# Kernel optimization log

Measured on AMD Instinct MI355X. Metric: run time of the kernel, lower is better.

The kernel has to match this reference:

```python
import jax, jax.numpy as jnp
import numpy as np

TOP_K = 4
N_GROUP = 8
TOPK_GROUP = 4
SCALE = 1.0

B, S, H, I, E = 2, 1024, 1024, 512, 32
SHARED_I = I * 2  # n_shared_experts = 2


def setup_inputs() -> dict:
    key = jax.random.key(0)
    ks = jax.random.split(key, 9)
    return {
        "hidden_states": jax.random.normal(ks[0], (B, S, H), jnp.float32),
        "gate_w": jax.random.normal(ks[1], (E, H), jnp.float32) * 0.02,
        "gate_bias": jnp.zeros((E,), jnp.float32),
        "gate_proj": jax.random.normal(ks[2], (E, I, H), jnp.float32) * 0.02,
        "up_proj": jax.random.normal(ks[3], (E, I, H), jnp.float32) * 0.02,
        "down_proj": jax.random.normal(ks[4], (E, H, I), jnp.float32) * 0.02,
        "shared_gate_w": jax.random.normal(ks[5], (SHARED_I, H), jnp.float32) * 0.02,
        "shared_up_w": jax.random.normal(ks[6], (SHARED_I, H), jnp.float32) * 0.02,
        "shared_down_w": jax.random.normal(ks[7], (H, SHARED_I), jnp.float32) * 0.02,
    }


def reference(hidden_states, gate_w, gate_bias, gate_proj, up_proj, down_proj,
              shared_gate_w, shared_up_w, shared_down_w):
    b, s, h = hidden_states.shape
    e = gate_w.shape[0]
    x = hidden_states.reshape(-1, h)            # (T, H)
    t = x.shape[0]

    # ---- gating (DeepSeek-V3 grouped sigmoid routing) ----
    logits = x @ gate_w.T                       # (T, E)
    scores = jax.nn.sigmoid(logits)
    sfc = scores + gate_bias[None, :]           # scores_for_choice
    # per-group score = sum of top-2 experts in group
    group_scores = jax.lax.top_k(sfc.reshape(t, N_GROUP, -1), 2)[0].sum(-1)  # (T, G)
    _, gidx = jax.lax.top_k(group_scores, TOPK_GROUP)                        # (T, topk_group)
    gmask = jax.nn.one_hot(gidx, N_GROUP, dtype=sfc.dtype).sum(1)            # (T, G)
    smask = jnp.repeat(gmask, e // N_GROUP, axis=1)                          # (T, E)
    tmp = jnp.where(smask > 0, sfc, 0.0)
    _, topk_idx = jax.lax.top_k(tmp, TOP_K)                                  # (T, K)
    topk_w = jnp.take_along_axis(scores, topk_idx, axis=1)                   # (T, K)
    topk_w = topk_w / (topk_w.sum(-1, keepdims=True) + 1e-20)                # norm_topk_prob
    topk_w = topk_w * SCALE

    # ---- routed experts (dense combine-weight formulation) ----
    comb = jnp.zeros((t, e), x.dtype).at[jnp.arange(t)[:, None], topk_idx].add(topk_w)  # (T, E)
    g = jnp.einsum('th,eih->eti', x, gate_proj)   # (E, T, I)
    u = jnp.einsum('th,eih->eti', x, up_proj)     # (E, T, I)
    a = jax.nn.silu(g) * u
    a = a * comb.T[:, :, None]                    # scale before down-proj to skip zero experts
    out = jnp.einsum('eti,ehi->th', a, down_proj) # (T, H)

    # ---- shared experts ----
    sg = x @ shared_gate_w.T
    su = x @ shared_up_w.T
    out = out + (jax.nn.silu(sg) * su) @ shared_down_w.T

    return out.reshape(b, s, h)
```

## Files before the change

kernel.cpp:

```cpp
#include <hip/hip_runtime.h>
#include <hip/hip_bf16.h>
#include <cstdint>
#include <cstddef>

#define H_DIM 1024
#define I_DIM 512
#define E_NUM 32
#define SHARED_I_DIM 1024
#define TOPK 4
#define NGROUP 8
#define TOPKG 4
#define GT 8

typedef __attribute__((ext_vector_type(8))) short bf16x8;
typedef __attribute__((ext_vector_type(4))) float f32x4;
typedef __attribute__((ext_vector_type(8))) unsigned short u16x8;

__device__ inline unsigned short f2bf(float f) {
    __hip_bfloat16 h = __float2bfloat16(f);
    return *reinterpret_cast<unsigned short*>(&h);
}
__device__ inline float bf2f(unsigned short u) {
    union { unsigned int u; float f; } w;
    w.u = ((unsigned int)u) << 16;
    return w.f;
}

__device__ inline int laddr(int row, int chunk) {
    return row * 32 + ((chunk ^ ((row >> 1) & 3)) << 3);
}

__global__ __launch_bounds__(256) void gate_kernel(const float* __restrict__ x,
                                                   const float* __restrict__ gw,
                                                   float* __restrict__ logits_out,
                                                   unsigned short* __restrict__ x_bf,
                                                   int* __restrict__ cnt) {
    int tb = blockIdx.x;
    int tid = threadIdx.x;
    if (tb == 0 && tid < 64) cnt[tid] = 0;
    __shared__ float xs[GT][H_DIM];
    __shared__ float ps[8][GT][E_NUM];
    const float* xsrc = x + (size_t)tb * GT * H_DIM;
    for (int i = tid; i < GT * H_DIM / 4; i += 256)
        ((float4*)&xs[0][0])[i] = ((const float4*)xsrc)[i];
    __syncthreads();
    {
        unsigned short* dst = x_bf + (size_t)tb * GT * H_DIM;
#pragma unroll
        for (int i = 0; i < GT * H_DIM / 8 / 256; ++i) {
            int idx = i * 256 + tid;
            const float* s = &xs[0][0] + idx * 8;
            u16x8 v;
            v[0] = f2bf(s[0]); v[1] = f2bf(s[1]); v[2] = f2bf(s[2]); v[3] = f2bf(s[3]);
            v[4] = f2bf(s[4]); v[5] = f2bf(s[5]); v[6] = f2bf(s[6]); v[7] = f2bf(s[7]);
            *(u16x8*)(dst + idx * 8) = v;
        }
    }
    int e = tid & 31, part = tid >> 5;
    const float* wrow = gw + (size_t)e * H_DIM + part * 128;
    float acc[GT] = {};
    for (int c0 = 0; c0 < 128; c0 += 32) {
        float w[32];
#pragma unroll
        for (int c = 0; c < 32; c++) w[c] = wrow[c0 + c];
#pragma unroll
        for (int t = 0; t < GT; t++) {
#pragma unroll
            for (int c = 0; c < 32; c++)
                acc[t] += w[c] * xs[t][part * 128 + c0 + c];
        }
    }
#pragma unroll
    for (int t = 0; t < GT; t++) ps[part][t][e] = acc[t];
    __syncthreads();
    {
        int t = tid >> 5, ee = tid & 31;
        float s = 0.f;
#pragma unroll
        for (int p = 0; p < 8; p++) s += ps[p][t][ee];
        logits_out[((size_t)tb * GT + t) * E_NUM + ee] = s;
    }
}

__global__ void select_kernel(const float* __restrict__ logits, const float* __restrict__ gb,
                              int* __restrict__ topk_e, float* __restrict__ topk_w,
                              int* __restrict__ cnt, int T) {
    int t = blockIdx.x * blockDim.x + threadIdx.x;
    if (t >= T) return;
    float scores[E_NUM], sfc[E_NUM];
#pragma unroll
    for (int i = 0; i < E_NUM; i++) {
        float l = logits[(size_t)t * E_NUM + i];
        float s = 1.f / (1.f + expf(-l));
        scores[i] = s;
        sfc[i] = s + gb[i];
    }
    float gs[NGROUP];
#pragma unroll
    for (int g = 0; g < NGROUP; g++) {
        float m1 = -1e30f, m2 = -1e30f;
#pragma unroll
        for (int j = 0; j < 4; j++) {
            float v = sfc[g * 4 + j];
            if (v > m1) { m2 = m1; m1 = v; }
            else if (v > m2) { m2 = v; }
        }
        gs[g] = m1 + m2;
    }
    unsigned gmask = 0;
    for (int r = 0; r < TOPKG; r++) {
        int best = 0; float bv = -1e30f;
#pragma unroll
        for (int g = 0; g < NGROUP; g++)
            if (!((gmask >> g) & 1u) && gs[g] > bv) { bv = gs[g]; best = g; }
        gmask |= 1u << best;
    }
    unsigned cmask = 0;
    int eidx[TOPK]; float ew[TOPK]; float sum = 0.f;
    for (int r = 0; r < TOPK; r++) {
        int best = 0; float bv = -1e30f; float bsc = 0.f;
#pragma unroll
        for (int i = 0; i < E_NUM; i++) {
            float v = ((gmask >> (i >> 2)) & 1u) ? sfc[i] : 0.0f;
            if (!((cmask >> i) & 1u) && v > bv) { bv = v; best = i; bsc = scores[i]; }
        }
        cmask |= 1u << best;
        eidx[r] = best; ew[r] = bsc; sum += bsc;
    }
    float inv = 1.f / (sum + 1e-20f);
#pragma unroll
    for (int k = 0; k < TOPK; k++) {
        topk_e[t * TOPK + k] = eidx[k];
        topk_w[t * TOPK + k] = ew[k] * inv;
        atomicAdd(&cnt[eidx[k]], 1);
    }
}

__global__ void scan_kernel(const int* __restrict__ cnt, int* __restrict__ off) {
    if (threadIdx.x == 0) {
        int a = 0;
        for (int e = 0; e < E_NUM; e++) { off[e] = a; a += cnt[e]; }
        off[E_NUM] = a;
    }
}

__global__ void bin_kernel(const int* __restrict__ topk_e, const float* __restrict__ topk_w,
                           const int* __restrict__ off, int* __restrict__ cnt2,
                           int* __restrict__ slot_token, float* __restrict__ slot_w,
                           int* __restrict__ slot_of, int total) {
    int i = blockIdx.x * blockDim.x + threadIdx.x;
    if (i >= total) return;
    int e = topk_e[i];
    float w = topk_w[i];
    int pos = atomicAdd(&cnt2[e], 1);
    int slot = off[e] + pos;
    slot_token[slot] = i >> 2;
    slot_w[slot] = w;
    slot_of[i] = slot;
}

__global__ __launch_bounds__(256) void combine_kernel(const unsigned short* __restrict__ out_slot,
                                                      const int* __restrict__ slot_of,
                                                      float* __restrict__ out) {
    int t = blockIdx.x;
    int h = threadIdx.x * 4;
    int s0 = slot_of[t * TOPK + 0], s1 = slot_of[t * TOPK + 1];
    int s2 = slot_of[t * TOPK + 2], s3 = slot_of[t * TOPK + 3];
    ushort4 a = *(const ushort4*)(out_slot + (size_t)s0 * H_DIM + h);
    ushort4 b = *(const ushort4*)(out_slot + (size_t)s1 * H_DIM + h);
    ushort4 c = *(const ushort4*)(out_slot + (size_t)s2 * H_DIM + h);
    ushort4 d = *(const ushort4*)(out_slot + (size_t)s3 * H_DIM + h);
    float4 o = *(float4*)(out + (size_t)t * H_DIM + h);
    o.x += bf2f(a.x) + bf2f(b.x) + bf2f(c.x) + bf2f(d.x);
    o.y += bf2f(a.y) + bf2f(b.y) + bf2f(c.y) + bf2f(d.y);
    o.z += bf2f(a.z) + bf2f(b.z) + bf2f(c.z) + bf2f(d.z);
    o.w += bf2f(a.w) + bf2f(b.w) + bf2f(c.w) + bf2f(d.w);
    *(float4*)(out + (size_t)t * H_DIM + h) = o;
}

template <bool STAGE1>
__global__ __launch_bounds__(512, 2) void moe_gemm(
    const unsigned short* __restrict__ Axr, const unsigned short* __restrict__ Axs,
    const float* __restrict__ B1r_, const float* __restrict__ B2r_,
    const float* __restrict__ B1s_, const float* __restrict__ B2s_,
    void* __restrict__ Dr, void* __restrict__ Ds,
    const int* __restrict__ slot_token, const float* __restrict__ slot_w,
    const int* __restrict__ cnt, const int* __restrict__ off_arr, int T) {
    constexpr bool DUAL = STAGE1;
    int e = blockIdx.x, itile = blockIdx.y, mtile = blockIdx.z;
    bool sh = (e == E_NUM);
    int NI = STAGE1 ? (sh ? 16 : 8) : 16;
    if (itile >= NI) return;
    int count = sh ? T : cnt[e];
    int base = sh ? 0 : off_arr[e];
    if (mtile * 256 >= count) return;
    const int K = STAGE1 ? H_DIM : (sh ? SHARED_I_DIM : I_DIM);

    __shared__ __align__(16) unsigned short As[2][256 * 32];
    __shared__ __align__(16) unsigned short Bs1[2][64 * 32];
    __shared__ __align__(16) unsigned short Bs2[2][DUAL ? 64 * 32 : 8];

    int tid = threadIdx.x, lane = tid & 63, wid = tid >> 6;

    int as_row = tid >> 1, as_c0 = (tid & 1) * 2;
    int am = mtile * 256 + as_row;
    int amc = (am < count) ? am : 0;
    const unsigned short* Abase;
    size_t arow;
    if constexpr (STAGE1) {
        Abase = Axr;
        arow = sh ? (size_t)amc : (size_t)slot_token[base + amc];
    } else {
        Abase = sh ? Axs : Axr;
        arow = sh ? (size_t)amc : (size_t)(base + amc);
    }
    const unsigned short* Ga = Abase + arow * K + as_c0 * 8;

    int bs_row = tid >> 3;
    int brow = itile * 64 + bs_row;
    int bwr = laddr(bs_row, (tid & 7) >> 1) + (tid & 1) * 4;
    const float* Gb1;
    const float* Gb2 = nullptr;
    if constexpr (STAGE1) {
        Gb1 = (sh ? B1s_ : (B1r_ + (size_t)e * (I_DIM * H_DIM))) + (size_t)brow * K + (tid & 7) * 4;
        Gb2 = (sh ? B2s_ : (B2r_ + (size_t)e * (I_DIM * H_DIM))) + (size_t)brow * K + (tid & 7) * 4;
    } else {
        Gb1 = (sh ? B1s_ : (B1r_ + (size_t)e * (H_DIM * I_DIM))) + (size_t)brow * K + (tid & 7) * 4;
    }

    f32x4 acc1[4][2] = {};
    f32x4 acc2[DUAL ? 4 : 1][2] = {};

    int wrow = (wid >> 1) * 64, wcol = (wid & 1) * 32;
    int frow = lane & 15, fch = lane >> 4;

    u16x8 a00, a01, a10, a11;
    float4 b10, b20, b11, b21;

    auto loadS = [&](u16x8& a0, u16x8& a1, float4& b1v, float4& b2v, int ks) {
        int k0 = ks << 5;
        a0 = *(const u16x8*)(Ga + k0);
        a1 = *(const u16x8*)(Ga + k0 + 8);
        b1v = *(const float4*)(Gb1 + k0);
        if constexpr (DUAL) b2v = *(const float4*)(Gb2 + k0);
    };
    auto writeS = [&](int buf, u16x8 a0, u16x8 a1, float4 b1v, float4 b2v) {
        *(u16x8*)(&As[buf][laddr(as_row, as_c0)]) = a0;
        *(u16x8*)(&As[buf][laddr(as_row, as_c0 + 1)]) = a1;
        ushort4 s;
        s.x = f2bf(b1v.x); s.y = f2bf(b1v.y); s.z = f2bf(b1v.z); s.w = f2bf(b1v.w);
        *(ushort4*)(&Bs1[buf][bwr]) = s;
        if constexpr (DUAL) {
            ushort4 s2;
            s2.x = f2bf(b2v.x); s2.y = f2bf(b2v.y); s2.z = f2bf(b2v.z); s2.w = f2bf(b2v.w);
            *(ushort4*)(&Bs2[buf][bwr]) = s2;
        }
    };
    auto compute = [&](int buf) {
        bf16x8 af[4], b1[2], b2[DUAL ? 2 : 1];
#pragma unroll
        for (int nf = 0; nf < 2; nf++)
            b1[nf] = *(const bf16x8*)(&Bs1[buf][laddr(wcol + nf * 16 + frow, fch)]);
        if constexpr (DUAL) {
#pragma unroll
            for (int nf = 0; nf < 2; nf++)
                b2[nf] = *(const bf16x8*)(&Bs2[buf][laddr(wcol + nf * 16 + frow, fch)]);
        }
#pragma unroll
        for (int mf = 0; mf < 4; mf++)
            af[mf] = *(const bf16x8*)(&As[buf][laddr(wrow + mf * 16 + frow, fch)]);
#pragma unroll
        for (int mf = 0; mf < 4; mf++)
#pragma unroll
            for (int nf = 0; nf < 2; nf++) {
                acc1[mf][nf] = __builtin_amdgcn_mfma_f32_16x16x32_bf16(af[mf], b1[nf], acc1[mf][nf], 0, 0, 0);
                if constexpr (DUAL)
                    acc2[mf][nf] = __builtin_amdgcn_mfma_f32_16x16x32_bf16(af[mf], b2[nf], acc2[mf][nf], 0, 0, 0);
            }
    };

    const int NK = K >> 5;
    loadS(a00, a01, b10, b20, 0);
    loadS(a10, a11, b11, b21, 1);
    writeS(0, a00, a01, b10, b20);
    loadS(a00, a01, b10, b20, 2);
    __syncthreads();
    for (int it = 0; it < NK; it += 2) {
        writeS(1, a10, a11, b11, b21);
        if (it + 3 < NK) loadS(a10, a11, b11, b21, it + 3);
        compute(0);
        __syncthreads();
        if (it + 2 < NK) {
            writeS(0, a00, a01, b10, b20);
            if (it + 4 < NK) loadS(a00, a01, b10, b20, it + 4);
        }
        compute(1);
        if (it + 2 < NK) __syncthreads();
    }

#pragma unroll
    for (int mf = 0; mf < 4; mf++)
#pragma unroll
        for (int nf = 0; nf < 2; nf++)
#pragma unroll
            for (int j = 0; j < 4; j++) {
                int rloc = wrow + mf * 16 + (lane >> 4) * 4 + j;
                int mrow = mtile * 256 + rloc;
                int col = itile * 64 + wcol + nf * 16 + (lane & 15);
                if (mrow >= count) continue;
                if constexpr (STAGE1) {
                    float w = sh ? 1.0f : slot_w[base + mrow];
                    float g = acc1[mf][nf][j];
                    float a = (g / (1.f + __expf(-g))) * acc2[mf][nf][j] * w;
                    if (sh) ((unsigned short*)Ds)[(size_t)mrow * SHARED_I_DIM + col] = f2bf(a);
                    else    ((unsigned short*)Dr)[(size_t)(base + mrow) * I_DIM + col] = f2bf(a);
                } else {
                    if (sh) ((float*)Ds)[(size_t)mrow * H_DIM + col] = acc1[mf][nf][j];
                    else    ((unsigned short*)Dr)[(size_t)(base + mrow) * H_DIM + col] = f2bf(acc1[mf][nf][j]);
                }
            }
}

extern "C" void kernel_launch(void* const* d_in, const int* in_sizes, int n_in,
                              void* d_out, int out_size, void* d_ws, size_t ws_size,
                              hipStream_t stream) {
    const float* x = (const float*)d_in[0];
    const float* gw = (const float*)d_in[1];
    const float* gb = (const float*)d_in[2];
    const float* gate_proj = (const float*)d_in[3];
    const float* up_proj = (const float*)d_in[4];
    const float* down_proj = (const float*)d_in[5];
    const float* sgw = (const float*)d_in[6];
    const float* suw = (const float*)d_in[7];
    const float* sdw = (const float*)d_in[8];
    float* out = (float*)d_out;

    const int T = in_sizes[0] / H_DIM;
    const int total_slots = T * TOPK;

    char* ws = (char*)d_ws;
    int* cnt = (int*)ws;
    int* cnt2 = cnt + 32;
    int* off = cnt + 64;
    int* topk_e = cnt + 128;
    float* topk_w = (float*)(topk_e + total_slots);
    int* slot_token = (int*)(topk_w + total_slots);
    float* slot_w = (float*)(slot_token + total_slots);
    int* slot_of = (int*)(slot_w + total_slots);
    float* logits = (float*)(slot_of + total_slots);
    unsigned short* x_bf = (unsigned short*)(logits + (size_t)T * E_NUM);
    unsigned short* act_r = x_bf + (size_t)T * H_DIM;
    unsigned short* act_s = act_r + (size_t)(total_slots + 256) * I_DIM;
    unsigned short* out_slot = act_s + (size_t)T * SHARED_I_DIM;

    hipLaunchKernelGGL(gate_kernel, dim3(T / GT), dim3(256), 0, stream,
                       x, gw, logits, x_bf, cnt);
    hipLaunchKernelGGL(select_kernel, dim3((T + 255) / 256), dim3(256), 0, stream,
                       logits, gb, topk_e, topk_w, cnt, T);
    hipLaunchKernelGGL(scan_kernel, dim3(1), dim3(1), 0, stream, cnt, off);
    hipLaunchKernelGGL(bin_kernel, dim3((total_slots + 255) / 256), dim3(256), 0, stream,
                       topk_e, topk_w, off, cnt2, slot_token, slot_w, slot_of, total_slots);

    hipLaunchKernelGGL((moe_gemm<true>), dim3(E_NUM + 1, 16, 32), dim3(512), 0, stream,
                       x_bf, (const unsigned short*)nullptr,
                       gate_proj, up_proj, sgw, suw,
                       (void*)act_r, (void*)act_s,
                       slot_token, slot_w, cnt, off, T);

    hipLaunchKernelGGL((moe_gemm<false>), dim3(E_NUM + 1, 16, 32), dim3(512), 0, stream,
                       act_r, act_s,
                       down_proj, (const float*)nullptr, sdw, (const float*)nullptr,
                       (void*)out_slot, (void*)out,
                       slot_token, slot_w, cnt, off, T);

    hipLaunchKernelGGL(combine_kernel, dim3(T), dim3(256), 0, stream, out_slot, slot_of, out);
}
```

Before: 189.7 us.

## Deepen register prefetch to four stages and use lightweight LDS barriers

The GEMM main loop now prefetches global tiles four k-steps ahead into four register sets, where it used two before, while still alternating between two LDS buffers. __syncthreads is replaced by an explicit lgkmcnt wait plus s_barrier, so the barrier does not wait on outstanding global loads (vmcnt). The aim is to hide global memory latency behind more MFMA work. In exchange, register pressure rises and occupancy may drop; the loop also assumes NK is a multiple of 4.

```diff
diff --git a/kernel.cpp b/kernel.cpp
--- a/kernel.cpp
+++ b/kernel.cpp
@@ -24,6 +24,11 @@
     union { unsigned int u; float f; } w;
     w.u = ((unsigned int)u) << 16;
     return w.f;
+}
+
+__device__ inline void bar_lds() {
+    asm volatile("s_waitcnt lgkmcnt(0)" ::: "memory");
+    __builtin_amdgcn_s_barrier();
 }
 
 __device__ inline int laddr(int row, int chunk) {
@@ -234,8 +239,8 @@
     int wrow = (wid >> 1) * 64, wcol = (wid & 1) * 32;
     int frow = lane & 15, fch = lane >> 4;
 
-    u16x8 a00, a01, a10, a11;
-    float4 b10, b20, b11, b21;
+    u16x8 aA0, aA1, aB0, aB1, aC0, aC1, aD0, aD1;
+    float4 bA1, bA2, bB1, bB2, bC1, bC2, bD1, bD2;
 
     auto loadS = [&](u16x8& a0, u16x8& a1, float4& b1v, float4& b2v, int ks) {
         int k0 = ks << 5;
@@ -280,22 +285,32 @@
     };
 
     const int NK = K >> 5;
-    loadS(a00, a01, b10, b20, 0);
-    loadS(a10, a11, b11, b21, 1);
-    writeS(0, a00, a01, b10, b20);
-    loadS(a00, a01, b10, b20, 2);
-    __syncthreads();
-    for (int it = 0; it < NK; it += 2) {
-        writeS(1, a10, a11, b11, b21);
-        if (it + 3 < NK) loadS(a10, a11, b11, b21, it + 3);
+    loadS(aA0, aA1, bA1, bA2, 0);
+    loadS(aB0, aB1, bB1, bB2, 1);
+    loadS(aC0, aC1, bC1, bC2, 2);
+    loadS(aD0, aD1, bD1, bD2, 3);
+    writeS(0, aA0, aA1, bA1, bA2);
+    if (4 < NK) loadS(aA0, aA1, bA1, bA2, 4);
+    bar_lds();
+    for (int it = 0; it < NK; it += 4) {
+        writeS(1, aB0, aB1, bB1, bB2);
+        if (it + 5 < NK) loadS(aB0, aB1, bB1, bB2, it + 5);
         compute(0);
-        __syncthreads();
-        if (it + 2 < NK) {
-            writeS(0, a00, a01, b10, b20);
-            if (it + 4 < NK) loadS(a00, a01, b10, b20, it + 4);
-        }
+        bar_lds();
+        writeS(0, aC0, aC1, bC1, bC2);
+        if (it + 6 < NK) loadS(aC0, aC1, bC1, bC2, it + 6);
         compute(1);
-        if (it + 2 < NK) __syncthreads();
+        bar_lds();
+        writeS(1, aD0, aD1, bD1, bD2);
+        if (it + 7 < NK) loadS(aD0, aD1, bD1, bD2, it + 7);
+        compute(0);
+        bar_lds();
+        if (it + 4 < NK) {
+            writeS(0, aA0, aA1, bA1, bA2);
+            if (it + 8 < NK) loadS(aA0, aA1, bA1, bA2, it + 8);
+        }
+        compute(1);
+        if (it + 4 < NK) bar_lds();
     }
 
 #pragma unroll
```

After: 195.8 us. 1.03x slower.
